# Optimization experiments

Measured on AMD Instinct MI355X. Metric: run time of the kernel, lower is better.

The kernel has to match this reference:

```python
import jax, jax.numpy as jnp
import numpy as np

B = 48            # graph pairs
NQ, NC = 20, 16   # query / corpus node counts (corpus padded to NMAX)
NMAX = 20         # max_node_set_size
DN, DE = 16, 8    # raw node / edge feature dims
D = 32            # node_state_dim
EH = 64           # edge_hidden_sizes[-1]
EQ, EC = 80, 60   # edges per query / corpus graph
PROP = 5          # n_prop_layers
TEMP = 0.01       # sinkhorn temperature
ITERS = 20        # sinkhorn iterations
LAMBDA = 1.0
NTOT = B * (NQ + NC)
NE = B * (EQ + EC)
SRC, DST = np.triu_indices(NMAX, 1)   # nC2 = 190 node pairs
_indq = np.ones(NMAX, np.int32)
_indc = np.array([1] * NC + [0] * (NMAX - NC), np.int32)
NXOR = jnp.asarray((_indq[:, None] ^ _indc[None, :]).astype(np.float32))  # [20,20]


def _mlp2(x, w1, b1, w2, b2):
    return jnp.maximum(x @ w1 + b1, 0.0) @ w2 + b2


def _sinkhorn(log_alpha):
    la = log_alpha / TEMP
    for _ in range(ITERS):
        la = la - jax.nn.logsumexp(la, axis=2, keepdims=True)
        la = la - jax.nn.logsumexp(la, axis=1, keepdims=True)
    return jnp.exp(la)


def _edge_emb(H, adj, w1, b1, w2, b2):
    s, d = H[:, SRC], H[:, DST]            # [B,nC2,D] gathers
    e = adj[:, SRC, DST][..., None]        # [B,nC2,1]
    f = _mlp2(jnp.concatenate([s, d, e], -1), w1, b1, w2, b2)
    bk = _mlp2(jnp.concatenate([d, s, e], -1), w1, b1, w2, b2)
    return f + bk                          # bidirectional msg, [B,nC2,EH]


def _forward(node_features, edge_features, query_adj, corpus_adj,
             enc_nw, enc_nb, enc_ew, enc_eb,
             msg_w1, msg_b1, msg_w2, msg_b2,
             upd_w1, upd_b1, upd_w2, upd_b2,
             sink_w1, sink_b1, sink_w2, sink_b2,
             lrl_w1, lrl_b1, lrl_w2, lrl_b2,
             from_idx, to_idx):
    h = node_features @ enc_nw + enc_nb    # GMN encoder (linear MLPs)
    e = edge_features @ enc_ew + enc_eb
    for _ in range(PROP):                  # shared-param propagation
        msg = _mlp2(jnp.concatenate([h[from_idx], h[to_idx], e], -1),
                    msg_w1, msg_b1, msg_w2, msg_b2)
        agg = jax.ops.segment_sum(msg, to_idx, num_segments=NTOT)
        h = h + _mlp2(jnp.concatenate([agg, h], -1), upd_w1, upd_b1, upd_w2, upd_b2)
    hp = h.reshape(B, NQ + NC, D)          # split_and_stack (static sizes)
    Hq = hp[:, :NQ]
    Hc = jnp.pad(hp[:, NQ:], ((0, 0), (0, NMAX - NC), (0, 0)))
    tq = _mlp2(Hq, sink_w1, sink_b1, sink_w2, sink_b2)
    tc = _mlp2(Hc, sink_w1, sink_b1, sink_w2, sink_b2)
    cost = jnp.abs(tq[:, :, None, :] - tc[:, None, :, :]).sum(-1)  # cdist p=1
    P = _sinkhorn(-cost)                   # node transport plan [B,20,20]
    Eq = _edge_emb(Hq, query_adj, lrl_w1, lrl_b1, lrl_w2, lrl_b2)
    Ec = _edge_emb(Hc, corpus_adj, lrl_w1, lrl_b1, lrl_w2, lrl_b2)
    Pa, Pb = P[:, SRC, :], P[:, DST, :]
    straight = Pa[:, :, SRC] * Pb[:, :, DST]    # plan[src_i,src_j]*plan[dst_i,dst_j]
    cross = Pa[:, :, DST] * Pb[:, :, SRC]
    eT = straight + cross                  # use_max=False, no second sinkhorn
    aq = query_adj[:, SRC, DST].astype(jnp.int32)
    ac = corpus_adj[:, SRC, DST].astype(jnp.int32)
    pxor = (aq[:, :, None] ^ ac[:, None, :]).astype(P.dtype)
    ediff = Eq[:, :, None, :] - Ec[:, None, :, :]   # [B,nC2,nC2,EH]
    ecost = jnp.maximum(ediff, 0.0).sum(-1) + jnp.maximum(-ediff, 0.0).sum(-1)
    edge_align = (pxor * eT * ecost).sum((-1, -2))
    ndiff = Hq[:, :, None, :] - Hc[:, None, :, :]   # [B,20,20,D]
    ncost = jnp.maximum(ndiff, 0.0).sum(-1) + jnp.maximum(-ndiff, 0.0).sum(-1)
    node_align = (NXOR * P * ncost).sum((-1, -2))
    return edge_align + LAMBDA * node_align         # [B]


def setup_inputs():
    key = jax.random.key(0)
    rng = np.random.default_rng(0)
    base = (np.arange(B) * (NQ + NC))[:, None]
    fq = base + rng.integers(0, NQ, (B, EQ)); tq = base + rng.integers(0, NQ, (B, EQ))
    fc = base + NQ + rng.integers(0, NC, (B, EC)); tc = base + NQ + rng.integers(0, NC, (B, EC))
    from_idx = jnp.asarray(np.concatenate([fq, fc], 1).reshape(-1), jnp.int32)
    to_idx = jnp.asarray(np.concatenate([tq, tc], 1).reshape(-1), jnp.int32)
    qadj = rng.integers(0, 2, (B, NMAX, NMAX)).astype(np.float32)
    cadj = rng.integers(0, 2, (B, NMAX, NMAX)).astype(np.float32)
    cadj[:, NC:, :] = 0.0; cadj[:, :, NC:] = 0.0   # padded corpus nodes have no edges
    ks = iter(jax.random.split(key, 32))
    def w(shape, s=0.1):
        return jax.random.normal(next(ks), shape, jnp.float32) * s
    return {
        'node_features': w((NTOT, DN), 1.0),
        'edge_features': w((NE, DE), 1.0),
        'query_adj': jnp.asarray(qadj),
        'corpus_adj': jnp.asarray(cadj),
        'enc_nw': w((DN, D)), 'enc_nb': w((D,)),
        'enc_ew': w((DE, 16)), 'enc_eb': w((16,)),
        'msg_w1': w((2 * D + 16, EH)), 'msg_b1': w((EH,)),
        'msg_w2': w((EH, EH)), 'msg_b2': w((EH,)),
        'upd_w1': w((EH + D, EH)), 'upd_b1': w((EH,)),
        'upd_w2': w((EH, D)), 'upd_b2': w((D,)),
        'sink_w1': w((D, NMAX)), 'sink_b1': w((NMAX,)),
        'sink_w2': w((NMAX, NMAX)), 'sink_b2': w((NMAX,)),
        'lrl_w1': w((2 * D + 1, EH)), 'lrl_b1': w((EH,)),
        'lrl_w2': w((EH, EH)), 'lrl_b2': w((EH,)),
        'from_idx': from_idx, 'to_idx': to_idx,
        'graph_sizes': jnp.asarray(np.tile([NQ, NC], B), jnp.int32),
    }


def reference(node_features, edge_features, query_adj, corpus_adj,
              enc_nw, enc_nb, enc_ew, enc_eb,
              msg_w1, msg_b1, msg_w2, msg_b2,
              upd_w1, upd_b1, upd_w2, upd_b2,
              sink_w1, sink_b1, sink_w2, sink_b2,
              lrl_w1, lrl_b1, lrl_w2, lrl_b2,
              from_idx, to_idx, graph_sizes):
    return _forward(node_features, edge_features, query_adj, corpus_adj,
                    enc_nw, enc_nb, enc_ew, enc_eb,
                    msg_w1, msg_b1, msg_w2, msg_b2,
                    upd_w1, upd_b1, upd_w2, upd_b2,
                    sink_w1, sink_b1, sink_w2, sink_b2,
                    lrl_w1, lrl_b1, lrl_w2, lrl_b2,
                    from_idx, to_idx)
```

## Files before the change

### kernel.cpp

```cpp
#include <hip/hip_runtime.h>


constexpr int kB    = 48;
constexpr int kNM   = 20;
constexpr int kD    = 32;
constexpr int kNP   = 190;
constexpr int kNTOT = 1728;
constexpr int kIters = 20;
constexpr float kInvT = 100.0f;

__device__ __forceinline__ void pair_sd(int p, int& s, int& d) {
    int row = 0, rem = p;
    #pragma unroll
    for (int r = 0; r < 19; ++r) {
        int len = 19 - r;
        if (rem < len) { row = r; break; }
        rem -= len;
    }
    s = row; d = row + 1 + rem;
}

__device__ __forceinline__ float bc(float v, int k) {
    return __int_as_float(__builtin_amdgcn_readlane(__float_as_int(v), k));
}

__device__ __forceinline__ void lse20(float (&r)[20]) {
    float m01 = fmaxf(r[0], r[1]),  m23 = fmaxf(r[2], r[3]),
          m45 = fmaxf(r[4], r[5]),  m67 = fmaxf(r[6], r[7]),
          m89 = fmaxf(r[8], r[9]),  mab = fmaxf(r[10], r[11]),
          mcd = fmaxf(r[12], r[13]), mef = fmaxf(r[14], r[15]),
          mgh = fmaxf(r[16], r[17]), mij = fmaxf(r[18], r[19]);
    float n0 = fmaxf(m01, m23), n1 = fmaxf(m45, m67), n2 = fmaxf(m89, mab),
          n3 = fmaxf(mcd, mef), n4 = fmaxf(mgh, mij);
    float m = fmaxf(fmaxf(fmaxf(n0, n1), fmaxf(n2, n3)), n4);
    float e[20];
    #pragma unroll
    for (int k = 0; k < 20; ++k) e[k] = __expf(r[k] - m);
    float s01 = e[0] + e[1],  s23 = e[2] + e[3],  s45 = e[4] + e[5],
          s67 = e[6] + e[7],  s89 = e[8] + e[9],  sab = e[10] + e[11],
          scd = e[12] + e[13], sef = e[14] + e[15], sgh = e[16] + e[17],
          sij = e[18] + e[19];
    float t0 = s01 + s23, t1 = s45 + s67, t2 = s89 + sab,
          t3 = scd + sef, t4 = sgh + sij;
    float s = ((t0 + t1) + (t2 + t3)) + t4;
    float l = m + __logf(s);
    #pragma unroll
    for (int k = 0; k < 20; ++k) r[k] -= l;
}

__global__ void k_enc(const float* __restrict__ nf, const float* __restrict__ nw,
                      const float* __restrict__ nb, const float* __restrict__ ef,
                      const float* __restrict__ ew, const float* __restrict__ eb,
                      float* __restrict__ h, float* __restrict__ ee,
                      float* __restrict__ agg, float* __restrict__ out) {
    int tid = blockIdx.x * 256 + threadIdx.x;
    int stride = gridDim.x * 256;
    for (int i = tid; i < kNTOT * 32; i += stride) {
        int n = i >> 5, c = i & 31;
        float acc = nb[c];
        const float* row = nf + n * 16;
        #pragma unroll
        for (int k = 0; k < 16; ++k) acc = fmaf(row[k], nw[k * 32 + c], acc);
        h[i] = acc;
    }
    for (int i = tid; i < 6720 * 16; i += stride) {
        int n = i >> 4, c = i & 15;
        float acc = eb[c];
        const float* row = ef + n * 8;
        #pragma unroll
        for (int k = 0; k < 8; ++k) acc = fmaf(row[k], ew[k * 16 + c], acc);
        ee[i] = acc;
    }
    for (int i = tid; i < kNTOT * 64; i += stride) agg[i] = 0.f;
    if (tid < kB) out[tid] = 0.f;
}

__global__ void __launch_bounds__(256)
k_msg(const float* __restrict__ h, const float* __restrict__ ee,
      const int* __restrict__ fidx, const int* __restrict__ tidx,
      const float* __restrict__ w1, const float* __restrict__ b1,
      const float* __restrict__ w2, const float* __restrict__ b2,
      float* __restrict__ agg) {
    int w = threadIdx.x >> 6, lane = threadIdx.x & 63;
    int e0 = (blockIdx.x * 4 + w) * 2;
    int toj[2]; float xa[2], xb[2], acc[2], o[2];
    #pragma unroll
    for (int j = 0; j < 2; ++j) {
        int e = e0 + j;
        int fr = fidx[e]; toj[j] = tidx[e];
        xa[j] = h[(lane < 32 ? fr : toj[j]) * kD + (lane & 31)];
        xb[j] = ee[e * 16 + (lane & 15)];
        acc[j] = b1[lane];
    }
    #pragma unroll
    for (int k = 0; k < 64; ++k) {
        float w1k = w1[k * 64 + lane];
        #pragma unroll
        for (int j = 0; j < 2; ++j) acc[j] = fmaf(bc(xa[j], k), w1k, acc[j]);
    }
    #pragma unroll
    for (int k = 0; k < 16; ++k) {
        float w1k = w1[(64 + k) * 64 + lane];
        #pragma unroll
        for (int j = 0; j < 2; ++j) acc[j] = fmaf(bc(xb[j], k), w1k, acc[j]);
    }
    #pragma unroll
    for (int j = 0; j < 2; ++j) { acc[j] = fmaxf(acc[j], 0.f); o[j] = b2[lane]; }
    #pragma unroll
    for (int k = 0; k < 64; ++k) {
        float w2k = w2[k * 64 + lane];
        #pragma unroll
        for (int j = 0; j < 2; ++j) o[j] = fmaf(bc(acc[j], k), w2k, o[j]);
    }
    #pragma unroll
    for (int j = 0; j < 2; ++j) atomicAdd(&agg[toj[j] * 64 + lane], o[j]);
}

__global__ void __launch_bounds__(256)
k_upd(float* __restrict__ h, float* __restrict__ agg,
      const float* __restrict__ w1, const float* __restrict__ b1,
      const float* __restrict__ w2, const float* __restrict__ b2) {
    int w = threadIdx.x >> 6, lane = threadIdx.x & 63;
    int n0 = (blockIdx.x * 4 + w) * 2;
    float xa[2], xb[2], acc[2], o[2];
    #pragma unroll
    for (int j = 0; j < 2; ++j) {
        int n = n0 + j;
        xa[j] = agg[n * 64 + lane];
        agg[n * 64 + lane] = 0.f;
        xb[j] = h[n * kD + (lane & 31)];
        acc[j] = b1[lane];
    }
    #pragma unroll
    for (int k = 0; k < 64; ++k) {
        float w1k = w1[k * 64 + lane];
        #pragma unroll
        for (int j = 0; j < 2; ++j) acc[j] = fmaf(bc(xa[j], k), w1k, acc[j]);
    }
    #pragma unroll
    for (int k = 0; k < 32; ++k) {
        float w1k = w1[(64 + k) * 64 + lane];
        #pragma unroll
        for (int j = 0; j < 2; ++j) acc[j] = fmaf(bc(xb[j], k), w1k, acc[j]);
    }
    #pragma unroll
    for (int j = 0; j < 2; ++j) { acc[j] = fmaxf(acc[j], 0.f); o[j] = b2[lane & 31]; }
    #pragma unroll
    for (int k = 0; k < 64; ++k) {
        float w2k = w2[k * 32 + (lane & 31)];
        #pragma unroll
        for (int j = 0; j < 2; ++j) o[j] = fmaf(bc(acc[j], k), w2k, o[j]);
    }
    if (lane < 32) {
        #pragma unroll
        for (int j = 0; j < 2; ++j) h[(n0 + j) * kD + lane] += o[j];
    }
}

__global__ void k_sink_t(const float* __restrict__ h,
                         const float* __restrict__ w1, const float* __restrict__ b1,
                         const float* __restrict__ w2, const float* __restrict__ b2,
                         float* __restrict__ Hq, float* __restrict__ Hc,
                         float* __restrict__ tq, float* __restrict__ tc) {
    __shared__ float xs[4][32];
    __shared__ float hs[4][20];
    int w = threadIdx.x >> 6, lane = threadIdx.x & 63;
    int id = blockIdx.x * 4 + w;
    int side = id / (kB * kNM);
    int rem  = id % (kB * kNM);
    int b = rem / kNM, i = rem % kNM;
    if (lane < 32) {
        float v;
        if (side == 0) v = h[(b * 36 + i) * kD + lane];
        else           v = (i < 16) ? h[(b * 36 + 20 + i) * kD + lane] : 0.f;
        (side ? Hc : Hq)[(b * kNM + i) * kD + lane] = v;
        xs[w][lane] = v;
    }
    __syncthreads();
    if (lane < kNM) {
        float acc = b1[lane];
        #pragma unroll
        for (int k = 0; k < kD; ++k) acc += xs[w][k] * w1[k * kNM + lane];
        hs[w][lane] = fmaxf(acc, 0.f);
    }
    __syncthreads();
    if (lane < kNM) {
        float o = b2[lane];
        #pragma unroll
        for (int k = 0; k < kNM; ++k) o += hs[w][k] * w2[k * kNM + lane];
        (side ? tc : tq)[(b * kNM + i) * kNM + lane] = o;
    }
}

__global__ void k_sinkhorn(const float* __restrict__ tq, const float* __restrict__ tc,
                           const float* __restrict__ Hq,
                           float* __restrict__ P, float* __restrict__ out) {
    __shared__ float tcS[400];
    __shared__ float tr[20 * 21];
    int b = blockIdx.x, lane = threadIdx.x;
    for (int i = lane; i < 400; i += 64) tcS[i] = tc[b * 400 + i];
    int i20 = lane < 20 ? lane : 0;
    float tqr[20];
    #pragma unroll
    for (int k = 0; k < 20; ++k) tqr[k] = tq[(b * 20 + i20) * 20 + k];
    __syncthreads();
    float r[20];
    #pragma unroll
    for (int j = 0; j < 20; ++j) {
        float c = 0.f;
        #pragma unroll
        for (int k = 0; k < 20; ++k) c += fabsf(tqr[k] - tcS[j * 20 + k]);
        r[j] = -c * kInvT;
    }
    for (int it = 0; it < kIters; ++it) {
        lse20(r);
        if (lane < 20) {
            #pragma unroll
            for (int j = 0; j < 20; ++j) tr[lane * 21 + j] = r[j];
        }
        __syncthreads();
        if (lane < 20) {
            #pragma unroll
            for (int i = 0; i < 20; ++i) r[i] = tr[i * 21 + lane];
        }
        __syncthreads();
        lse20(r);
        if (lane < 20) {
            #pragma unroll
            for (int i = 0; i < 20; ++i) tr[i * 21 + lane] = r[i];
        }
        __syncthreads();
        if (lane < 20) {
            #pragma unroll
            for (int j = 0; j < 20; ++j) r[j] = tr[lane * 21 + j];
        }
        __syncthreads();
    }
    float part = 0.f;
    if (lane < 20) {
        float pv[20];
        #pragma unroll
        for (int j = 0; j < 20; ++j) pv[j] = __expf(r[j]);
        float* Pb = P + b * 400 + lane * 20;
        #pragma unroll
        for (int j = 0; j < 20; ++j) Pb[j] = pv[j];
        float pr4 = (pv[16] + pv[17]) + (pv[18] + pv[19]);
        float l1 = 0.f;
        const float* hq = Hq + (b * 20 + lane) * 32;
        #pragma unroll
        for (int k = 0; k < 32; ++k) l1 += fabsf(hq[k]);
        part = pr4 * l1;
    }
    #pragma unroll
    for (int off = 32; off; off >>= 1) part += __shfl_down(part, off, 64);
    if (lane == 0) atomicAdd(&out[b], part);
}

__global__ void __launch_bounds__(256)
k_edge_emb(const float* __restrict__ Hq, const float* __restrict__ Hc,
           const float* __restrict__ qadj, const float* __restrict__ cadj,
           const float* __restrict__ w1, const float* __restrict__ b1,
           const float* __restrict__ w2, const float* __restrict__ b2,
           float* __restrict__ Eq, float* __restrict__ Ec) {
    int w = threadIdx.x >> 6, lane = threadIdx.x & 63;
    int id0 = (blockIdx.x * 4 + w) * 4;
    float xa[4], ev[4], af[4], ab[4];
    int sidej[4], bj[4], pj[4];
    #pragma unroll
    for (int j = 0; j < 4; ++j) {
        int id = id0 + j;
        sidej[j] = id / (kB * kNP);
        int rem  = id % (kB * kNP);
        bj[j] = rem / kNP; pj[j] = rem % kNP;
        int s, d; pair_sd(pj[j], s, d);
        const float* H = sidej[j] ? Hc : Hq;
        xa[j] = (lane < 32) ? H[(bj[j] * kNM + s) * kD + lane]
                            : H[(bj[j] * kNM + d) * kD + (lane - 32)];
        ev[j] = (sidej[j] ? cadj : qadj)[bj[j] * 400 + s * 20 + d];
        float bb = b1[lane];
        af[j] = bb; ab[j] = bb;
    }
    #pragma unroll
    for (int k = 0; k < 64; ++k) {
        float w1k = w1[k * 64 + lane];
        #pragma unroll
        for (int j = 0; j < 4; ++j) {
            af[j] = fmaf(bc(xa[j], k),      w1k, af[j]);
            ab[j] = fmaf(bc(xa[j], k ^ 32), w1k, ab[j]);
        }
    }
    {
        float w1e = w1[64 * 64 + lane];
        #pragma unroll
        for (int j = 0; j < 4; ++j) {
            af[j] = fmaf(ev[j], w1e, af[j]);
            ab[j] = fmaf(ev[j], w1e, ab[j]);
        }
    }
    float hid[4], o[4];
    #pragma unroll
    for (int j = 0; j < 4; ++j) {
        hid[j] = fmaxf(af[j], 0.f) + fmaxf(ab[j], 0.f);
        o[j] = 2.f * b2[lane];
    }
    #pragma unroll
    for (int k = 0; k < 64; ++k) {
        float w2k = w2[k * 64 + lane];
        #pragma unroll
        for (int j = 0; j < 4; ++j) o[j] = fmaf(bc(hid[j], k), w2k, o[j]);
    }
    #pragma unroll
    for (int j = 0; j < 4; ++j)
        (sidej[j] ? Ec : Eq)[(bj[j] * kNP + pj[j]) * 64 + lane] = o[j];
}

__global__ void __launch_bounds__(1024, 1)
k_final(const float* __restrict__ P, const float* __restrict__ Eq,
        const float* __restrict__ Ec, const float* __restrict__ qadj,
        const float* __restrict__ cadj, float* __restrict__ out) {
    __shared__ float Ps[400];
    __shared__ unsigned char spsh[192], dpsh[192];
    int b = blockIdx.x / 6, qt = blockIdx.x % 6;
    int t = threadIdx.x, w = t >> 6, lane = t & 63;

    float ec[32];
    #pragma unroll
    for (int j = 0; j < 32; ++j) {
        int qq = qt * 32 + j;
        ec[j] = (qq < kNP) ? Ec[(b * kNP + qq) * 64 + lane] : 0.f;
    }
    if (t < 192) {
        int s = 0, d = 0;
        if (t < kNP) pair_sd(t, s, d);
        spsh[t] = (unsigned char)s;
        dpsh[t] = (unsigned char)d;
    }
    if (t < 400) Ps[t] = P[b * 400 + t];
    __syncthreads();

    int l31 = lane & 31;
    int q = qt * 32 + l31;
    bool qv = q < kNP;
    int sq = spsh[qv ? q : 0], dq = dpsh[qv ? q : 0];
    float acv = qv ? cadj[b * 400 + sq * 20 + dq] : 0.f;

    float a0 = 0.f, a1 = 0.f, a2 = 0.f, a3 = 0.f;
    for (int pp = w; pp < kNP; pp += 16) {
        int sp = spsh[pp], dp = dpsh[pp];
        float aq = qadj[b * 400 + sp * 20 + dp];
        float eT = Ps[sp * 20 + sq] * Ps[dp * 20 + dq]
                 + Ps[sp * 20 + dq] * Ps[dp * 20 + sq];
        float wqv = qv ? ((aq > 0.5f) ? (1.f - acv) : acv) * eT : 0.f;
        float eqv = Eq[(b * kNP + pp) * 64 + lane];
        #pragma unroll
        for (int j = 0; j < 32; j += 4) {
            a0 = fmaf(bc(wqv, j + 0), fabsf(eqv - ec[j + 0]), a0);
            a1 = fmaf(bc(wqv, j + 1), fabsf(eqv - ec[j + 1]), a1);
            a2 = fmaf(bc(wqv, j + 2), fabsf(eqv - ec[j + 2]), a2);
            a3 = fmaf(bc(wqv, j + 3), fabsf(eqv - ec[j + 3]), a3);
        }
    }
    float partial = (a0 + a1) + (a2 + a3);
    #pragma unroll
    for (int off = 32; off; off >>= 1) partial += __shfl_down(partial, off, 64);
    if (lane == 0) atomicAdd(&out[b], partial);
}

extern "C" void kernel_launch(void* const* d_in, const int* in_sizes, int n_in,
                              void* d_out, int out_size, void* d_ws, size_t ws_size,
                              hipStream_t stream) {
    auto f = [&](int i) { return (const float*)d_in[i]; };
    const float* nf   = f(0);
    const float* ef   = f(1);
    const float* qadj = f(2);
    const float* cadj = f(3);
    const int* from_idx = (const int*)d_in[24];
    const int* to_idx   = (const int*)d_in[25];
    float* out = (float*)d_out;

    float* ws  = (float*)d_ws;
    float* h   = ws;
    float* ee  = h   + 55296;
    float* agg = ee  + 107520;
    float* Hq  = agg + 110592;
    float* Hc  = Hq  + 30720;
    float* tq  = Hc  + 30720;
    float* tc  = tq  + 19200;
    float* P   = tc  + 19200;
    float* Eq  = P   + 19200;
    float* Ec  = Eq  + 583680;

    k_enc<<<432, 256, 0, stream>>>(nf, f(4), f(5), ef, f(6), f(7), h, ee, agg, out);
    for (int it = 0; it < 5; ++it) {
        k_msg<<<840, 256, 0, stream>>>(h, ee, from_idx, to_idx,
                                       f(8), f(9), f(10), f(11), agg);
        k_upd<<<216, 256, 0, stream>>>(h, agg, f(12), f(13), f(14), f(15));
    }
    k_sink_t<<<480, 256, 0, stream>>>(h, f(16), f(17), f(18), f(19), Hq, Hc, tq, tc);
    k_sinkhorn<<<48, 64, 0, stream>>>(tq, tc, Hq, P, out);
    k_edge_emb<<<1140, 256, 0, stream>>>(Hq, Hc, qadj, cadj,
                                         f(20), f(21), f(22), f(23), Eq, Ec);
    k_final<<<288, 1024, 0, stream>>>(P, Eq, Ec, qadj, cadj, out);
}
```

Measured before the change: 164.7 us.

## Remap blocks per XCD by batch and shrink final kernel to 256-thread blocks

Block indices in the sinkhorn-transform, edge-embedding and final kernels are remapped so that each XCD handles whole batch items, aiming for better L2 locality of per-graph data. The final kernel moves from 1024-thread to 256-thread blocks, with each wave covering more pair rows. Its loop software-prefetches the next Eq row and adjacency value. The trade-off is fewer resident waves per (batch, tile) in the final kernel, which lengthens each wave's serial loop in exchange for higher occupancy per CU.

```diff
diff --git a/kernel.cpp b/kernel.cpp
--- a/kernel.cpp
+++ b/kernel.cpp
@@ -165,10 +165,11 @@
     __shared__ float xs[4][32];
     __shared__ float hs[4][20];
     int w = threadIdx.x >> 6, lane = threadIdx.x & 63;
-    int id = blockIdx.x * 4 + w;
-    int side = id / (kB * kNM);
-    int rem  = id % (kB * kNM);
-    int b = rem / kNM, i = rem % kNM;
+    int xcd = blockIdx.x & 7, slot = blockIdx.x >> 3;
+    int b = xcd + 8 * (slot / 10);
+    int task = (slot % 10) * 4 + w;
+    int side = task >= 20;
+    int i = task - side * 20;
     if (lane < 32) {
         float v;
         if (side == 0) v = h[(b * 36 + i) * kD + lane];
@@ -263,20 +264,21 @@
            const float* __restrict__ w2, const float* __restrict__ b2,
            float* __restrict__ Eq, float* __restrict__ Ec) {
     int w = threadIdx.x >> 6, lane = threadIdx.x & 63;
-    int id0 = (blockIdx.x * 4 + w) * 4;
+    int xcd = blockIdx.x & 7, slot = blockIdx.x >> 3;
+    int b = xcd + 8 * (slot / 24);
+    int r = slot % 24;
     float xa[4], ev[4], af[4], ab[4];
-    int sidej[4], bj[4], pj[4];
+    int sidej[4], pj[4];
     #pragma unroll
     for (int j = 0; j < 4; ++j) {
-        int id = id0 + j;
-        sidej[j] = id / (kB * kNP);
-        int rem  = id % (kB * kNP);
-        bj[j] = rem / kNP; pj[j] = rem % kNP;
+        int tloc = r * 16 + w * 4 + j;
+        if (tloc >= 380) tloc = 379;
+        sidej[j] = tloc / kNP; pj[j] = tloc % kNP;
         int s, d; pair_sd(pj[j], s, d);
         const float* H = sidej[j] ? Hc : Hq;
-        xa[j] = (lane < 32) ? H[(bj[j] * kNM + s) * kD + lane]
-                            : H[(bj[j] * kNM + d) * kD + (lane - 32)];
-        ev[j] = (sidej[j] ? cadj : qadj)[bj[j] * 400 + s * 20 + d];
+        xa[j] = (lane < 32) ? H[(b * kNM + s) * kD + lane]
+                            : H[(b * kNM + d) * kD + (lane - 32)];
+        ev[j] = (sidej[j] ? cadj : qadj)[b * 400 + s * 20 + d];
         float bb = b1[lane];
         af[j] = bb; ab[j] = bb;
     }
@@ -311,31 +313,25 @@
     }
     #pragma unroll
     for (int j = 0; j < 4; ++j)
-        (sidej[j] ? Ec : Eq)[(bj[j] * kNP + pj[j]) * 64 + lane] = o[j];
-}
-
-__global__ void __launch_bounds__(1024, 1)
+        (sidej[j] ? Ec : Eq)[(b * kNP + pj[j]) * 64 + lane] = o[j];
+}
+
+__global__ void __launch_bounds__(256, 4)
 k_final(const float* __restrict__ P, const float* __restrict__ Eq,
         const float* __restrict__ Ec, const float* __restrict__ qadj,
         const float* __restrict__ cadj, float* __restrict__ out) {
     __shared__ float Ps[400];
     __shared__ unsigned char spsh[192], dpsh[192];
-    int b = blockIdx.x / 6, qt = blockIdx.x % 6;
+    int xcd = blockIdx.x & 7, slot = blockIdx.x >> 3;
+    int b = xcd + 8 * (slot / 6), qt = slot % 6;
     int t = threadIdx.x, w = t >> 6, lane = t & 63;
-
-    float ec[32];
-    #pragma unroll
-    for (int j = 0; j < 32; ++j) {
-        int qq = qt * 32 + j;
-        ec[j] = (qq < kNP) ? Ec[(b * kNP + qq) * 64 + lane] : 0.f;
-    }
     if (t < 192) {
         int s = 0, d = 0;
         if (t < kNP) pair_sd(t, s, d);
         spsh[t] = (unsigned char)s;
         dpsh[t] = (unsigned char)d;
     }
-    if (t < 400) Ps[t] = P[b * 400 + t];
+    for (int i = t; i < 400; i += 256) Ps[i] = P[b * 400 + i];
     __syncthreads();
 
     int l31 = lane & 31;
@@ -344,21 +340,36 @@
     int sq = spsh[qv ? q : 0], dq = dpsh[qv ? q : 0];
     float acv = qv ? cadj[b * 400 + sq * 20 + dq] : 0.f;
 
+    float ec[32];
+    #pragma unroll
+    for (int j = 0; j < 32; ++j) {
+        int qq = qt * 32 + j;
+        ec[j] = (qq < kNP) ? Ec[(b * kNP + qq) * 64 + lane] : 0.f;
+    }
+
     float a0 = 0.f, a1 = 0.f, a2 = 0.f, a3 = 0.f;
-    for (int pp = w; pp < kNP; pp += 16) {
+    int pp = w;
+    float aqc = qadj[b * 400 + spsh[pp] * 20 + dpsh[pp]];
+    float eqc = Eq[(b * kNP + pp) * 64 + lane];
+    while (pp < kNP) {
+        int pn = pp + 4;
+        float aqn = 0.f, eqn = 0.f;
+        if (pn < kNP) {
+            aqn = qadj[b * 400 + spsh[pn] * 20 + dpsh[pn]];
+            eqn = Eq[(b * kNP + pn) * 64 + lane];
+        }
         int sp = spsh[pp], dp = dpsh[pp];
-        float aq = qadj[b * 400 + sp * 20 + dp];
         float eT = Ps[sp * 20 + sq] * Ps[dp * 20 + dq]
                  + Ps[sp * 20 + dq] * Ps[dp * 20 + sq];
-        float wqv = qv ? ((aq > 0.5f) ? (1.f - acv) : acv) * eT : 0.f;
-        float eqv = Eq[(b * kNP + pp) * 64 + lane];
+        float wqv = qv ? ((aqc > 0.5f) ? (1.f - acv) : acv) * eT : 0.f;
         #pragma unroll
         for (int j = 0; j < 32; j += 4) {
-            a0 = fmaf(bc(wqv, j + 0), fabsf(eqv - ec[j + 0]), a0);
-            a1 = fmaf(bc(wqv, j + 1), fabsf(eqv - ec[j + 1]), a1);
-            a2 = fmaf(bc(wqv, j + 2), fabsf(eqv - ec[j + 2]), a2);
-            a3 = fmaf(bc(wqv, j + 3), fabsf(eqv - ec[j + 3]), a3);
-        }
+            a0 = fmaf(bc(wqv, j + 0), fabsf(eqc - ec[j + 0]), a0);
+            a1 = fmaf(bc(wqv, j + 1), fabsf(eqc - ec[j + 1]), a1);
+            a2 = fmaf(bc(wqv, j + 2), fabsf(eqc - ec[j + 2]), a2);
+            a3 = fmaf(bc(wqv, j + 3), fabsf(eqc - ec[j + 3]), a3);
+        }
+        aqc = aqn; eqc = eqn; pp = pn;
     }
     float partial = (a0 + a1) + (a2 + a3);
     #pragma unroll
@@ -398,7 +409,7 @@
     }
     k_sink_t<<<480, 256, 0, stream>>>(h, f(16), f(17), f(18), f(19), Hq, Hc, tq, tc);
     k_sinkhorn<<<48, 64, 0, stream>>>(tq, tc, Hq, P, out);
-    k_edge_emb<<<1140, 256, 0, stream>>>(Hq, Hc, qadj, cadj,
+    k_edge_emb<<<1152, 256, 0, stream>>>(Hq, Hc, qadj, cadj,
                                          f(20), f(21), f(22), f(23), Eq, Ec);
-    k_final<<<288, 1024, 0, stream>>>(P, Eq, Ec, qadj, cadj, out);
-}
+    k_final<<<288, 256, 0, stream>>>(P, Eq, Ec, qadj, cadj, out);
+}
```

Result: faster. 152.1 us (-7.6%).
